# Performance work log

Measured on AMD Instinct MI355X. Metric: run time of the kernel, lower is better.

The kernel has to match this reference:

```python
import jax, jax.numpy as jnp
import numpy as np


def setup_inputs() -> dict:
    key = jax.random.key(0)
    k1, k2 = jax.random.split(key)
    N, C, H, W = 4, 128, 160, 320
    left = jax.random.normal(k1, (N, C, H, W), dtype=jnp.float32)
    right = jax.random.normal(k2, (N, C, H, W), dtype=jnp.float32)
    return {"left": left, "right": right, "max_disparity": 48}


def reference(left, right, max_disparity):
    # left, right: (N, C, H, W) -> volume: (N, D, H, W)
    # volume[n, d, h, w] = sum_c left[n, c, h, w] * right[n, c, h, w - d]  (0 if w < d)
    n, c, h, w = left.shape
    slices = []
    for d in range(max_disparity):  # fixed structural constant, unrolled at trace time
        # channel dot-product of overlapping strips, shape (N, H, W - d)
        corr = jnp.einsum('nchw,nchw->nhw', left[:, :, :, d:], right[:, :, :, :w - d])
        # left-pad the first d columns with zeros to restore width W
        slices.append(jnp.pad(corr, ((0, 0), (0, 0), (d, 0))))
    return jnp.stack(slices, axis=1)  # (N, D, H, W)
```

## Files before the change

### kernel.cpp

```cpp
#include <hip/hip_runtime.h>


#define NN 4
#define CC 128
#define HH 160
#define WW 320
#define DD 48
#define HWs (HH * WW)
#define WB 160
#define RROWS 208
#define RPITCH 68
#define RTASKS 3328

typedef _Float16 h2 __attribute__((ext_vector_type(2)));
typedef _Float16 f16x8 __attribute__((ext_vector_type(8)));
typedef float f32x4 __attribute__((ext_vector_type(4)));
typedef __fp16 h2raw __attribute__((ext_vector_type(2)));

__device__ __forceinline__ h2 pack2(float a, float b) {
  union { h2raw r; h2 h; } u;
  u.r = __builtin_amdgcn_cvt_pkrtz(a, b);
  return u.h;
}

__global__ __launch_bounds__(640)
void corr_kernel(const float* __restrict__ L, const float* __restrict__ R,
                 float* __restrict__ out) {
  __shared__ __align__(16) h2 Rh[RROWS][RPITCH];

  const int tid = threadIdx.x;
  const int wt  = tid >> 6;
  const int ln  = tid & 63;
  const int i16 = ln & 15;
  const int g   = ln >> 4;

  const int bid = blockIdx.x;
  const int wsplit = bid & 1;
  const int row_nh = bid >> 1;
  const int n = row_nh / HH;
  const int h = row_nh - n * HH;
  const int wb = wsplit * WB;

  const size_t base = (size_t)n * CC * HWs + (size_t)h * WW;
  const float* Rbase = R + base;
  const float* Lbase = L + base + wb + 16 * wt + i16;

  union F4 { float4 f; float a[4]; };
  F4 ra[6], rc[6];
#pragma unroll
  for (int it = 0; it < 6; ++it) {
    int t = tid + it * 640;
    ra[it].f = make_float4(0.f, 0.f, 0.f, 0.f);
    rc[it].f = make_float4(0.f, 0.f, 0.f, 0.f);
    if (t < RTASKS) {
      int c2 = t / 52, v = t - 52 * c2;
      int col = wb - 48 + 4 * v;
      if (col >= 0) {
        const float* p = Rbase + (size_t)(2 * c2) * HWs + col;
        ra[it].f = *(const float4*)p;
        rc[it].f = *(const float4*)(p + HWs);
      }
    }
  }

  float lv[32];
#pragma unroll
  for (int ks = 0; ks < 4; ++ks)
#pragma unroll
    for (int e = 0; e < 8; ++e)
      lv[ks * 8 + e] = Lbase[(size_t)(32 * ks + 8 * g + e) * HWs];

#pragma unroll
  for (int it = 0; it < 6; ++it) {
    int t = tid + it * 640;
    if (t < RTASKS) {
      int c2 = t / 52, v = t - 52 * c2;
      int colp = c2 ^ (4 * (v & 7));
#pragma unroll
      for (int i = 0; i < 4; ++i)
        Rh[4 * v + i][colp] = pack2(ra[it].a[i], rc[it].a[i]);
    }
  }

  union AU { f16x8 v; h2 h[4]; };
  AU A[4];
#pragma unroll
  for (int ks = 0; ks < 4; ++ks)
#pragma unroll
    for (int j = 0; j < 4; ++j)
      A[ks].h[j] = pack2(lv[ks * 8 + 2 * j], lv[ks * 8 + 2 * j + 1]);

  __syncthreads();

  f32x4 acc[4] = {};
#pragma unroll
  for (int q = 0; q < 4; ++q) {
    const int row = 16 * (wt + q) + i16;
    const int swz = 4 * ((row >> 2) & 7);
    union BU { float4 f; f16x8 v; } B;
#pragma unroll
    for (int ks = 0; ks < 4; ++ks) {
      B.f = *(const float4*)&Rh[row][(16 * ks + 4 * g) ^ swz];
      acc[q] = __builtin_amdgcn_mfma_f32_16x16x32_f16(A[ks].v, B.v, acc[q], 0, 0, 0);
    }
  }

  __syncthreads();

  float* Ep = ((float*)&Rh[0][0]) + wt * (DD * 20);
#pragma unroll
  for (int q = 0; q < 4; ++q)
#pragma unroll
    for (int r = 0; r < 4; ++r) {
      int d = 48 - 16 * q + 4 * g + r - i16;
      if (d >= 0 && d < DD) Ep[d * 20 + 4 * g + r] = acc[q][r];
    }

  const int l4 = ln & 3;
  const int dr = ln >> 2;
  float* outp = out + (size_t)n * DD * HWs + (size_t)h * WW + wb + 16 * wt + 4 * l4;
#pragma unroll
  for (int rr = 0; rr < 3; ++rr) {
    int d = 16 * rr + dr;
    float4 val = *(const float4*)&Ep[d * 20 + 4 * l4];
    *(float4*)&outp[(size_t)d * HWs] = val;
  }
}

extern "C" void kernel_launch(void* const* d_in, const int* in_sizes, int n_in,
                              void* d_out, int out_size, void* d_ws, size_t ws_size,
                              hipStream_t stream) {
  const float* L = (const float*)d_in[0];
  const float* R = (const float*)d_in[1];
  float* out = (float*)d_out;
  corr_kernel<<<dim3(2 * NN * HH), dim3(640), 0, stream>>>(L, R, out);
}
```

Baseline: 236.1 us.

## Split width into four blocks and store R channel-major in shared memory

Each block now covers 80 output columns with 320 threads instead of 160 columns with 640 threads, and twice as many blocks are launched. Shared memory for R is now laid out channel-pair-major, so staging becomes one contiguous float4 store per task. The MFMA B operands are then gathered as four scalar h2 reads, replacing the swizzled vector read. The aim is more resident blocks for better occupancy and simpler staging, at the cost of more halo reloads of R per output column and more LDS read instructions in the MFMA loop.

```diff
diff --git a/kernel.cpp b/kernel.cpp
--- a/kernel.cpp
+++ b/kernel.cpp
@@ -7,10 +7,11 @@
 #define WW 320
 #define DD 48
 #define HWs (HH * WW)
-#define WB 160
-#define RROWS 208
-#define RPITCH 68
-#define RTASKS 3328
+#define WB 80
+#define RROWS 128
+#define RPITCH 132
+#define RTASKS 2048
+#define NTHREADS 320
 
 typedef _Float16 h2 __attribute__((ext_vector_type(2)));
 typedef _Float16 f16x8 __attribute__((ext_vector_type(8)));
@@ -23,10 +24,10 @@
   return u.h;
 }
 
-__global__ __launch_bounds__(640)
+__global__ __launch_bounds__(NTHREADS, 5)
 void corr_kernel(const float* __restrict__ L, const float* __restrict__ R,
                  float* __restrict__ out) {
-  __shared__ __align__(16) h2 Rh[RROWS][RPITCH];
+  __shared__ __align__(16) h2 Rh[64][RPITCH];
 
   const int tid = threadIdx.x;
   const int wt  = tid >> 6;
@@ -35,8 +36,8 @@
   const int g   = ln >> 4;
 
   const int bid = blockIdx.x;
-  const int wsplit = bid & 1;
-  const int row_nh = bid >> 1;
+  const int wsplit = bid & 3;
+  const int row_nh = bid >> 2;
   const int n = row_nh / HH;
   const int h = row_nh - n * HH;
   const int wb = wsplit * WB;
@@ -46,14 +47,14 @@
   const float* Lbase = L + base + wb + 16 * wt + i16;
 
   union F4 { float4 f; float a[4]; };
-  F4 ra[6], rc[6];
+  F4 ra[7], rc[7];
 #pragma unroll
-  for (int it = 0; it < 6; ++it) {
-    int t = tid + it * 640;
+  for (int it = 0; it < 7; ++it) {
+    int t = tid + it * NTHREADS;
     ra[it].f = make_float4(0.f, 0.f, 0.f, 0.f);
     rc[it].f = make_float4(0.f, 0.f, 0.f, 0.f);
     if (t < RTASKS) {
-      int c2 = t / 52, v = t - 52 * c2;
+      int c2 = t >> 5, v = t & 31;
       int col = wb - 48 + 4 * v;
       if (col >= 0) {
         const float* p = Rbase + (size_t)(2 * c2) * HWs + col;
@@ -70,15 +71,16 @@
     for (int e = 0; e < 8; ++e)
       lv[ks * 8 + e] = Lbase[(size_t)(32 * ks + 8 * g + e) * HWs];
 
+  union V4 { float4 f; h2 h[4]; };
 #pragma unroll
-  for (int it = 0; it < 6; ++it) {
-    int t = tid + it * 640;
+  for (int it = 0; it < 7; ++it) {
+    int t = tid + it * NTHREADS;
     if (t < RTASKS) {
-      int c2 = t / 52, v = t - 52 * c2;
-      int colp = c2 ^ (4 * (v & 7));
+      int c2 = t >> 5, v = t & 31;
+      V4 u;
 #pragma unroll
-      for (int i = 0; i < 4; ++i)
-        Rh[4 * v + i][colp] = pack2(ra[it].a[i], rc[it].a[i]);
+      for (int i = 0; i < 4; ++i) u.h[i] = pack2(ra[it].a[i], rc[it].a[i]);
+      *(float4*)&Rh[c2][4 * v] = u.f;
     }
   }
 
@@ -95,12 +97,13 @@
   f32x4 acc[4] = {};
 #pragma unroll
   for (int q = 0; q < 4; ++q) {
-    const int row = 16 * (wt + q) + i16;
-    const int swz = 4 * ((row >> 2) & 7);
-    union BU { float4 f; f16x8 v; } B;
+    const int j = 16 * (wt + q) + i16;
+    union BU { f16x8 v; h2 h[4]; } B;
 #pragma unroll
     for (int ks = 0; ks < 4; ++ks) {
-      B.f = *(const float4*)&Rh[row][(16 * ks + 4 * g) ^ swz];
+      const int r0 = 16 * ks + 4 * g;
+#pragma unroll
+      for (int r = 0; r < 4; ++r) B.h[r] = Rh[r0 + r][j];
       acc[q] = __builtin_amdgcn_mfma_f32_16x16x32_f16(A[ks].v, B.v, acc[q], 0, 0, 0);
     }
   }
@@ -133,5 +136,5 @@
   const float* L = (const float*)d_in[0];
   const float* R = (const float*)d_in[1];
   float* out = (float*)d_out;
-  corr_kernel<<<dim3(2 * NN * HH), dim3(640), 0, stream>>>(L, R, out);
+  corr_kernel<<<dim3(4 * NN * HH), dim3(NTHREADS), 0, stream>>>(L, R, out);
 }
```

New measurement: 244.7 us. 1.04x slower.

## Drop shared R staging; load R fragments per wave directly from global

Applied to the files above, without the earlier changes.

Each wave now loads its own right-image fragments straight from global memory into registers for every disparity block, instead of cooperatively staging a half-row of R into shared memory as fp16. Blocks shrink to 256 threads covering 64 columns, the grid grows to 3200 blocks with an XCD-aware block remap, and shared memory holds only the epilogue transpose buffer. The goal is to remove the block-wide barrier and the LDS staging cost and to raise occupancy. In exchange, each R element is fetched by several waves (up to four times), which adds global and L2 traffic.

```diff
diff --git a/kernel.cpp b/kernel.cpp
--- a/kernel.cpp
+++ b/kernel.cpp
@@ -7,10 +7,8 @@
 #define WW 320
 #define DD 48
 #define HWs (HH * WW)
-#define WB 160
-#define RROWS 208
-#define RPITCH 68
-#define RTASKS 3328
+#define NTH 256
+#define GRID 3200
 
 typedef _Float16 h2 __attribute__((ext_vector_type(2)));
 typedef _Float16 f16x8 __attribute__((ext_vector_type(8)));
@@ -23,107 +21,87 @@
   return u.h;
 }
 
-__global__ __launch_bounds__(640)
+__global__ __launch_bounds__(NTH, 4)
 void corr_kernel(const float* __restrict__ L, const float* __restrict__ R,
                  float* __restrict__ out) {
-  __shared__ __align__(16) h2 Rh[RROWS][RPITCH];
+  __shared__ __align__(16) float Ep[4][DD * 20];
 
   const int tid = threadIdx.x;
-  const int wt  = tid >> 6;
+  const int wid = tid >> 6;
   const int ln  = tid & 63;
   const int i16 = ln & 15;
   const int g   = ln >> 4;
 
-  const int bid = blockIdx.x;
-  const int wsplit = bid & 1;
-  const int row_nh = bid >> 1;
-  const int n = row_nh / HH;
-  const int h = row_nh - n * HH;
-  const int wb = wsplit * WB;
+  const int hwb = blockIdx.x;
+  const int bid = (hwb & 7) * (GRID / 8) + (hwb >> 3);
+
+  const int row = bid / 5;
+  const int grp = bid - 5 * row;
+  const int n = row / HH;
+  const int h = row - n * HH;
+  const int w0 = 64 * grp + 16 * wid;
 
   const size_t base = (size_t)n * CC * HWs + (size_t)h * WW;
-  const float* Rbase = R + base;
-  const float* Lbase = L + base + wb + 16 * wt + i16;
+  const float* Lp = L + base + w0 + i16;
+  const float* Rp = R + base + i16;
 
-  union F4 { float4 f; float a[4]; };
-  F4 ra[6], rc[6];
-#pragma unroll
-  for (int it = 0; it < 6; ++it) {
-    int t = tid + it * 640;
-    ra[it].f = make_float4(0.f, 0.f, 0.f, 0.f);
-    rc[it].f = make_float4(0.f, 0.f, 0.f, 0.f);
-    if (t < RTASKS) {
-      int c2 = t / 52, v = t - 52 * c2;
-      int col = wb - 48 + 4 * v;
-      if (col >= 0) {
-        const float* p = Rbase + (size_t)(2 * c2) * HWs + col;
-        ra[it].f = *(const float4*)p;
-        rc[it].f = *(const float4*)(p + HWs);
-      }
-    }
-  }
+  union AU { f16x8 v; h2 h[4]; };
 
-  float lv[32];
+  float la[32];
 #pragma unroll
   for (int ks = 0; ks < 4; ++ks)
 #pragma unroll
     for (int e = 0; e < 8; ++e)
-      lv[ks * 8 + e] = Lbase[(size_t)(32 * ks + 8 * g + e) * HWs];
-
-#pragma unroll
-  for (int it = 0; it < 6; ++it) {
-    int t = tid + it * 640;
-    if (t < RTASKS) {
-      int c2 = t / 52, v = t - 52 * c2;
-      int colp = c2 ^ (4 * (v & 7));
-#pragma unroll
-      for (int i = 0; i < 4; ++i)
-        Rh[4 * v + i][colp] = pack2(ra[it].a[i], rc[it].a[i]);
-    }
-  }
-
-  union AU { f16x8 v; h2 h[4]; };
+      la[ks * 8 + e] = Lp[(size_t)(32 * ks + 8 * g + e) * HWs];
   AU A[4];
 #pragma unroll
   for (int ks = 0; ks < 4; ++ks)
 #pragma unroll
     for (int j = 0; j < 4; ++j)
-      A[ks].h[j] = pack2(lv[ks * 8 + 2 * j], lv[ks * 8 + 2 * j + 1]);
+      A[ks].h[j] = pack2(la[ks * 8 + 2 * j], la[ks * 8 + 2 * j + 1]);
 
-  __syncthreads();
+  f32x4 acc[4];
+#pragma unroll
+  for (int q = 0; q < 4; ++q) acc[q] = (f32x4){0.f, 0.f, 0.f, 0.f};
 
-  f32x4 acc[4] = {};
 #pragma unroll
   for (int q = 0; q < 4; ++q) {
-    const int row = 16 * (wt + q) + i16;
-    const int swz = 4 * ((row >> 2) & 7);
-    union BU { float4 f; f16x8 v; } B;
+    const int j0 = w0 - 48 + 16 * q;
+    const bool ok = (j0 >= 0);
+    const float* rp = Rp + (ok ? j0 : 0);
+    float rb[32];
+#pragma unroll
+    for (int ks = 0; ks < 4; ++ks)
+#pragma unroll
+      for (int e = 0; e < 8; ++e)
+        rb[ks * 8 + e] = rp[(size_t)(32 * ks + 8 * g + e) * HWs];
+    const h2 z = pack2(0.f, 0.f);
 #pragma unroll
     for (int ks = 0; ks < 4; ++ks) {
-      B.f = *(const float4*)&Rh[row][(16 * ks + 4 * g) ^ swz];
+      AU B;
+#pragma unroll
+      for (int j = 0; j < 4; ++j)
+        B.h[j] = ok ? pack2(rb[ks * 8 + 2 * j], rb[ks * 8 + 2 * j + 1]) : z;
       acc[q] = __builtin_amdgcn_mfma_f32_16x16x32_f16(A[ks].v, B.v, acc[q], 0, 0, 0);
     }
   }
 
-  __syncthreads();
-
-  float* Ep = ((float*)&Rh[0][0]) + wt * (DD * 20);
+  float* ep = Ep[wid];
 #pragma unroll
   for (int q = 0; q < 4; ++q)
 #pragma unroll
     for (int r = 0; r < 4; ++r) {
       int d = 48 - 16 * q + 4 * g + r - i16;
-      if (d >= 0 && d < DD) Ep[d * 20 + 4 * g + r] = acc[q][r];
+      if (d >= 0 && d < DD) ep[d * 20 + 4 * g + r] = acc[q][r];
     }
 
   const int l4 = ln & 3;
   const int dr = ln >> 2;
-  float* outp = out + (size_t)n * DD * HWs + (size_t)h * WW + wb + 16 * wt + 4 * l4;
+  float* op = out + (size_t)n * DD * HWs + (size_t)h * WW + w0 + 4 * l4;
 #pragma unroll
   for (int rr = 0; rr < 3; ++rr) {
     int d = 16 * rr + dr;
-    float4 val = *(const float4*)&Ep[d * 20 + 4 * l4];
-    *(float4*)&outp[(size_t)d * HWs] = val;
+    *(float4*)&op[(size_t)d * HWs] = *(const float4*)&ep[d * 20 + 4 * l4];
   }
 }
 
@@ -133,5 +111,5 @@
   const float* L = (const float*)d_in[0];
   const float* R = (const float*)d_in[1];
   float* out = (float*)d_out;
-  corr_kernel<<<dim3(2 * NN * HH), dim3(640), 0, stream>>>(L, R, out);
+  corr_kernel<<<dim3(GRID), dim3(NTH), 0, stream>>>(L, R, out);
 }
```

New measurement: 287.1 us. 1.22x slower.
